# Kernel optimization log

Measured on AMD Instinct MI355X. Metric: run time of the kernel, lower is better.

Reference implementation:

```python
import jax, jax.numpy as jnp
import numpy as np

B, S, D, H = 8, 1024, 1024, 16
DK = D // H


def setup_inputs() -> dict:
    key = jax.random.key(0)
    ks = jax.random.split(key, 12)
    sc = 1.0 / np.sqrt(D)
    return {
        "query": jax.random.normal(ks[0], (B, S, D), jnp.float32),
        "key": jax.random.normal(ks[1], (B, S, D), jnp.float32),
        "value": jax.random.normal(ks[2], (B, S, D), jnp.float32),
        "Wq": jax.random.normal(ks[3], (D, D), jnp.float32) * sc,
        "bq": jnp.zeros((D,), jnp.float32),
        "Wk": jax.random.normal(ks[4], (D, D), jnp.float32) * sc,
        "bk": jnp.zeros((D,), jnp.float32),
        "Wv": jax.random.normal(ks[5], (D, D), jnp.float32) * sc,
        "bv": jnp.zeros((D,), jnp.float32),
        "Wa": jax.random.normal(ks[6], (D, D), jnp.float32) * sc,
        "ba": jnp.zeros((D,), jnp.float32),
        "qvec": jax.random.normal(ks[7], (D,), jnp.float32),
    }


def reference(query, key, value, Wq, bq, Wk, bk, Wv, bv, Wa, ba, qvec):
    # project and split heads: [B,S,D] -> [B,H,S,DK]
    def split(x, W, b):
        y = x @ W.T + b
        return y.reshape(B, S, H, DK).transpose(0, 2, 1, 3)

    q = split(query, Wq, bq)
    k = split(key, Wk, bk)
    v = split(value, Wv, bv)

    scores = jnp.einsum('bhqd,bhkd->bhqk', q, k) / jnp.sqrt(jnp.float32(DK))
    p = jax.nn.softmax(scores, axis=-1)          # dropout p=0 -> identity
    x = jnp.einsum('bhqk,bhkd->bhqd', p, v)
    x = x.transpose(0, 2, 1, 3).reshape(B, S, D)  # [B,S,D]

    # attention2 pooling head
    a = jnp.tanh(x @ Wa.T + ba) @ qvec           # [B,S]
    alpha = jax.nn.softmax(a, axis=-1)
    return jnp.einsum('bs,bsd->bd', alpha, x)    # [B,D]
```

## Files before the change

kernel.cpp:

```cpp
#include <hip/hip_runtime.h>

typedef __bf16 bf16;
typedef __attribute__((ext_vector_type(8))) __bf16 bf16x8;
typedef __attribute__((ext_vector_type(4))) __bf16 bf16x4;
typedef __attribute__((ext_vector_type(4))) float f32x4;

#define GLDS16(g, l) __builtin_amdgcn_global_load_lds( \
    (const __attribute__((address_space(1))) void*)(g), \
    (__attribute__((address_space(3))) void*)(l), 16, 0, 0)

#define MFMA16(a, b, c) __builtin_amdgcn_mfma_f32_16x16x32_bf16(a, b, c, 0, 0, 0)

#define TR16(dst, addr, off) \
  asm volatile("ds_read_b64_tr_b16 %0, %1 offset:" #off : "=v"(dst) : "v"(addr))

__global__ __launch_bounds__(256) void f2b_kernel(const float* __restrict__ in,
                                                  bf16* __restrict__ out, int n8) {
  int i = blockIdx.x * 256 + threadIdx.x;
  if (i >= n8) return;
  const f32x4* p = (const f32x4*)in + (size_t)i * 2;
  f32x4 a = p[0], b = p[1];
  bf16x8 o;
  o[0] = (bf16)a[0]; o[1] = (bf16)a[1]; o[2] = (bf16)a[2]; o[3] = (bf16)a[3];
  o[4] = (bf16)b[0]; o[5] = (bf16)b[1]; o[6] = (bf16)b[2]; o[7] = (bf16)b[3];
  ((bf16x8*)out)[i] = o;
}

template <int EPI>
__global__ __launch_bounds__(256) void gemm_bt(
    const bf16* __restrict__ A, const bf16* __restrict__ Bw,
    const float* __restrict__ bias, const float* __restrict__ qv,
    bf16* __restrict__ C, float* __restrict__ aout,
    int M, int N, int K) {
  __shared__ __attribute__((aligned(16))) bf16 As[4096];
  __shared__ __attribute__((aligned(16))) bf16 Bs[4096];
  const int tid = threadIdx.x;
  const int wid = tid >> 6, lane = tid & 63;
  const int g = lane >> 4, lc = lane & 15;
  const int row0 = blockIdx.x * 128, col0 = blockIdx.y * 128;
  const int wr = wid >> 1, wc = wid & 1;

  const int c0 = tid, c1 = tid + 256;
  const bf16* gA0 = A + ((size_t)(row0 + (c0 & 127)) * K + (c0 >> 7) * 8);
  const bf16* gA1 = A + ((size_t)(row0 + (c1 & 127)) * K + (c1 >> 7) * 8);
  const bf16* gB0 = Bw + ((size_t)(col0 + (c0 & 127)) * K + (c0 >> 7) * 8);
  const bf16* gB1 = Bw + ((size_t)(col0 + (c1 & 127)) * K + (c1 >> 7) * 8);
  bf16* lA0 = As + (size_t)(0 + wid * 64) * 8;
  bf16* lA1 = As + (size_t)(256 + wid * 64) * 8;
  bf16* lB0 = Bs + (size_t)(0 + wid * 64) * 8;
  bf16* lB1 = Bs + (size_t)(256 + wid * 64) * 8;

  const f32x4 z4 = {0.f, 0.f, 0.f, 0.f};
  f32x4 acc[4][4];
#pragma unroll
  for (int m = 0; m < 4; ++m)
#pragma unroll
    for (int n = 0; n < 4; ++n) acc[m][n] = z4;

  for (int kt = 0; kt < K; kt += 32) {
    GLDS16(gA0 + kt, lA0);
    GLDS16(gA1 + kt, lA1);
    GLDS16(gB0 + kt, lB0);
    GLDS16(gB1 + kt, lB1);
    __syncthreads();
    bf16x8 af[4], bfv[4];
#pragma unroll
    for (int m = 0; m < 4; ++m)
      af[m] = *(const bf16x8*)(As + g * 1024 + (wr * 64 + m * 16 + lc) * 8);
#pragma unroll
    for (int n = 0; n < 4; ++n)
      bfv[n] = *(const bf16x8*)(Bs + g * 1024 + (wc * 64 + n * 16 + lc) * 8);
#pragma unroll
    for (int m = 0; m < 4; ++m)
#pragma unroll
      for (int n = 0; n < 4; ++n)
        acc[m][n] = MFMA16(af[m], bfv[n], acc[m][n]);
    __syncthreads();
  }

  if constexpr (EPI == 0) {
#pragma unroll
    for (int n = 0; n < 4; ++n) {
      const int col = col0 + wc * 64 + n * 16 + lc;
      const float bb = bias[col];
#pragma unroll
      for (int m = 0; m < 4; ++m)
#pragma unroll
        for (int r = 0; r < 4; ++r) {
          const int row = row0 + wr * 64 + m * 16 + g * 4 + r;
          C[(size_t)row * N + col] = (bf16)(acc[m][n][r] + bb);
        }
    }
  } else {
    float part[4][4];
#pragma unroll
    for (int m = 0; m < 4; ++m)
#pragma unroll
      for (int r = 0; r < 4; ++r) part[m][r] = 0.f;
#pragma unroll
    for (int n = 0; n < 4; ++n) {
      const int col = col0 + wc * 64 + n * 16 + lc;
      const float bb = bias[col];
      const float qq = qv[col];
#pragma unroll
      for (int m = 0; m < 4; ++m)
#pragma unroll
        for (int r = 0; r < 4; ++r)
          part[m][r] += tanhf(acc[m][n][r] + bb) * qq;
    }
#pragma unroll
    for (int m = 0; m < 4; ++m)
#pragma unroll
      for (int r = 0; r < 4; ++r) {
        float v = part[m][r];
        v += __shfl_xor(v, 1); v += __shfl_xor(v, 2);
        v += __shfl_xor(v, 4); v += __shfl_xor(v, 8);
        if (lc == 0) {
          const int row = row0 + wr * 64 + m * 16 + g * 4 + r;
          atomicAdd(&aout[row], v);
        }
      }
  }
}

__global__ __launch_bounds__(256) void attn_kernel(
    const bf16* __restrict__ qp, const bf16* __restrict__ kp,
    const bf16* __restrict__ vp, bf16* __restrict__ xb, float* __restrict__ xf) {
  constexpr int S = 1024, D = 1024;
  __shared__ __attribute__((aligned(16))) bf16 Ks[4096];
  __shared__ __attribute__((aligned(16))) bf16 Vs[4096];
  __shared__ __attribute__((aligned(16))) bf16 Ps[4096];
  const int tid = threadIdx.x, wid = tid >> 6, lane = tid & 63;
  const int g = lane >> 4, lc = lane & 15;
  const int b = blockIdx.x >> 4, h = blockIdx.x & 15;
  const int q0 = blockIdx.y * 64;
  const size_t base = (size_t)b * S * D + (size_t)h * 64;

  bf16x8 qf[2];
  {
    const bf16* qrow = qp + base + (size_t)(q0 + wid * 16 + lc) * D;
    qf[0] = *(const bf16x8*)(qrow + g * 8);
    qf[1] = *(const bf16x8*)(qrow + 32 + g * 8);
#pragma unroll
    for (int j = 0; j < 8; ++j) {
      qf[0][j] = (bf16)((float)qf[0][j] * 0.125f);
      qf[1][j] = (bf16)((float)qf[1][j] * 0.125f);
    }
  }
  float m_s = -1e30f, l_s = 0.f;
  const f32x4 z4 = {0.f, 0.f, 0.f, 0.f};
  f32x4 ax[4];
#pragma unroll
  for (int m = 0; m < 4; ++m) ax[m] = z4;

  const int c0 = tid, c1 = tid + 256;
  const bf16* gK0 = kp + base + (size_t)(c0 & 63) * D + (c0 >> 6) * 8;
  const bf16* gK1 = kp + base + (size_t)(c1 & 63) * D + (c1 >> 6) * 8;
  bf16* lK0 = Ks + (size_t)(c0 - lane) * 8;
  bf16* lK1 = Ks + (size_t)(c1 - lane) * 8;
  const bf16* gV0 = vp + base + (size_t)((c0 >> 5) * 4 + ((c0 >> 1) & 3)) * D +
                    ((c0 >> 3) & 3) * 16 + (c0 & 1) * 8;
  const bf16* gV1 = vp + base + (size_t)((c1 >> 5) * 4 + ((c1 >> 1) & 3)) * D +
                    ((c1 >> 3) & 3) * 16 + (c1 & 1) * 8;
  bf16* lV0 = Vs + (size_t)(c0 - lane) * 8;
  bf16* lV1 = Vs + (size_t)(c1 - lane) * 8;

  bf16* pw = Ps + wid * 1024;
  const int pswz_a = lc & 3, pswz_b = (lc >> 2) & 3;
  const unsigned vaddr =
      (unsigned)(uintptr_t)(const __attribute__((address_space(3))) bf16*)(Vs + 512 * g + 4 * lc);

  for (int s0 = 0; s0 < S; s0 += 64) {
    __syncthreads();
    GLDS16(gK0 + (size_t)s0 * D, lK0);
    GLDS16(gK1 + (size_t)s0 * D, lK1);
    GLDS16(gV0 + (size_t)s0 * D, lV0);
    GLDS16(gV1 + (size_t)s0 * D, lV1);
    __syncthreads();

    f32x4 sc[4];
#pragma unroll
    for (int m = 0; m < 4; ++m) {
      f32x4 z = z4;
      bf16x8 kf0 = *(const bf16x8*)(Ks + (size_t)g * 512 + (m * 16 + lc) * 8);
      bf16x8 kf1 = *(const bf16x8*)(Ks + (size_t)(4 + g) * 512 + (m * 16 + lc) * 8);
      z = MFMA16(kf0, qf[0], z);
      z = MFMA16(kf1, qf[1], z);
      sc[m] = z;
    }
    float mx = -1e30f;
#pragma unroll
    for (int m = 0; m < 4; ++m)
      mx = fmaxf(mx, fmaxf(fmaxf(sc[m][0], sc[m][1]), fmaxf(sc[m][2], sc[m][3])));
    mx = fmaxf(mx, __shfl_xor(mx, 16));
    mx = fmaxf(mx, __shfl_xor(mx, 32));
    const float mn = fmaxf(m_s, mx);
    float sm = 0.f;
#pragma unroll
    for (int m = 0; m < 4; ++m)
#pragma unroll
      for (int r = 0; r < 4; ++r) {
        float p = __expf(sc[m][r] - mn);
        sc[m][r] = p;
        sm += p;
      }
    sm += __shfl_xor(sm, 16);
    sm += __shfl_xor(sm, 32);
    const float cr = __expf(m_s - mn);
    l_s = l_s * cr + sm;
    m_s = mn;

#pragma unroll
    for (int m = 0; m < 4; ++m) {
      bf16x4 pk;
      pk[0] = (bf16)sc[m][0]; pk[1] = (bf16)sc[m][1];
      pk[2] = (bf16)sc[m][2]; pk[3] = (bf16)sc[m][3];
      *(bf16x4*)(pw + lc * 64 + 16 * (m ^ pswz_a) + 4 * (g ^ pswz_b)) = pk;
    }
#pragma unroll
    for (int m = 0; m < 4; ++m) ax[m] *= cr;

    bf16x4 pr[2][2];
#pragma unroll
    for (int kk = 0; kk < 2; ++kk)
#pragma unroll
      for (int jh = 0; jh < 2; ++jh) {
        const int msrc = 2 * kk + (g >> 1);
        const int gsrc = (2 * g + jh) & 3;
        pr[kk][jh] = *(const bf16x4*)(pw + lc * 64 + 16 * (msrc ^ pswz_a) + 4 * (gsrc ^ pswz_b));
      }
    bf16x8 pf0 = __builtin_shufflevector(pr[0][0], pr[0][1], 0, 1, 2, 3, 4, 5, 6, 7);
    bf16x8 pf1 = __builtin_shufflevector(pr[1][0], pr[1][1], 0, 1, 2, 3, 4, 5, 6, 7);

    bf16x4 vt[4][2][2];
    TR16(vt[0][0][0], vaddr, 0);    TR16(vt[1][0][0], vaddr, 128);
    TR16(vt[2][0][0], vaddr, 256);  TR16(vt[3][0][0], vaddr, 384);
    TR16(vt[0][0][1], vaddr, 512);  TR16(vt[1][0][1], vaddr, 640);
    TR16(vt[2][0][1], vaddr, 768);  TR16(vt[3][0][1], vaddr, 896);
    TR16(vt[0][1][0], vaddr, 4096); TR16(vt[1][1][0], vaddr, 4224);
    TR16(vt[2][1][0], vaddr, 4352); TR16(vt[3][1][0], vaddr, 4480);
    TR16(vt[0][1][1], vaddr, 4608); TR16(vt[1][1][1], vaddr, 4736);
    TR16(vt[2][1][1], vaddr, 4864); TR16(vt[3][1][1], vaddr, 4992);
    asm volatile("s_waitcnt lgkmcnt(0)" ::: "memory");
    __builtin_amdgcn_sched_barrier(0);

#pragma unroll
    for (int md = 0; md < 4; ++md) {
      bf16x8 a0 = __builtin_shufflevector(vt[md][0][0], vt[md][0][1], 0, 1, 2, 3, 4, 5, 6, 7);
      bf16x8 a1 = __builtin_shufflevector(vt[md][1][0], vt[md][1][1], 0, 1, 2, 3, 4, 5, 6, 7);
      ax[md] = MFMA16(a0, pf0, ax[md]);
      ax[md] = MFMA16(a1, pf1, ax[md]);
    }
  }

  const float inv = 1.0f / l_s;
  const int qrow = q0 + wid * 16 + lc;
  float* xfr = xf + base + (size_t)qrow * D;
  bf16* xbr = xb + base + (size_t)qrow * D;
#pragma unroll
  for (int m = 0; m < 4; ++m)
#pragma unroll
    for (int r = 0; r < 4; ++r) {
      const int col = 16 * m + 4 * g + r;
      const float v = ax[m][r] * inv;
      xbr[col] = (bf16)v;
      xfr[col] = v;
    }
}

__global__ __launch_bounds__(256) void softmax_rows(const float* __restrict__ av,
                                                    float* __restrict__ alpha) {
  const int b = blockIdx.x, t = threadIdx.x;
  __shared__ float red[8];
  f32x4 v = *(const f32x4*)(av + b * 1024 + t * 4);
  float m = fmaxf(fmaxf(v[0], v[1]), fmaxf(v[2], v[3]));
#pragma unroll
  for (int o = 1; o < 64; o <<= 1) m = fmaxf(m, __shfl_xor(m, o));
  if ((t & 63) == 0) red[t >> 6] = m;
  __syncthreads();
  m = fmaxf(fmaxf(red[0], red[1]), fmaxf(red[2], red[3]));
  f32x4 e;
  float s = 0.f;
#pragma unroll
  for (int j = 0; j < 4; ++j) { e[j] = __expf(v[j] - m); s += e[j]; }
#pragma unroll
  for (int o = 1; o < 64; o <<= 1) s += __shfl_xor(s, o);
  if ((t & 63) == 0) red[4 + (t >> 6)] = s;
  __syncthreads();
  const float inv = 1.0f / (red[4] + red[5] + red[6] + red[7]);
  *(f32x4*)(alpha + b * 1024 + t * 4) = e * inv;
}

__global__ __launch_bounds__(256) void pool_kernel(const float* __restrict__ xf,
                                                   const float* __restrict__ alpha,
                                                   float* __restrict__ out) {
  const int b = blockIdx.y, sc = blockIdx.x, t = threadIdx.x;
  f32x4 acc = {0.f, 0.f, 0.f, 0.f};
  const float* xrow = xf + (size_t)b * 1024 * 1024;
  for (int s = sc * 64; s < sc * 64 + 64; ++s) {
    const float al = alpha[b * 1024 + s];
    f32x4 xv = *(const f32x4*)(xrow + (size_t)s * 1024 + t * 4);
    acc += xv * al;
  }
  atomicAdd(&out[b * 1024 + t * 4 + 0], acc[0]);
  atomicAdd(&out[b * 1024 + t * 4 + 1], acc[1]);
  atomicAdd(&out[b * 1024 + t * 4 + 2], acc[2]);
  atomicAdd(&out[b * 1024 + t * 4 + 3], acc[3]);
}

extern "C" void kernel_launch(void* const* d_in, const int* in_sizes, int n_in,
                              void* d_out, int out_size, void* d_ws, size_t ws_size,
                              hipStream_t stream) {
  const float* Q   = (const float*)d_in[0];
  const float* K   = (const float*)d_in[1];
  const float* V   = (const float*)d_in[2];
  const float* Wq  = (const float*)d_in[3];
  const float* bq  = (const float*)d_in[4];
  const float* Wk  = (const float*)d_in[5];
  const float* bk  = (const float*)d_in[6];
  const float* Wv  = (const float*)d_in[7];
  const float* bv  = (const float*)d_in[8];
  const float* Wa  = (const float*)d_in[9];
  const float* ba  = (const float*)d_in[10];
  const float* qvec = (const float*)d_in[11];
  float* out = (float*)d_out;
  char* ws = (char*)d_ws;
  const size_t MB = 1ull << 20;

  bf16* Wqb = (bf16*)(ws + 0 * MB);
  bf16* Wkb = (bf16*)(ws + 2 * MB);
  bf16* Wvb = (bf16*)(ws + 4 * MB);
  bf16* Wab = (bf16*)(ws + 6 * MB);
  bf16* qb  = (bf16*)(ws + 8 * MB);
  bf16* kb  = (bf16*)(ws + 24 * MB);
  bf16* vb  = (bf16*)(ws + 40 * MB);
  bf16* qp  = (bf16*)(ws + 56 * MB);
  bf16* kp  = (bf16*)(ws + 72 * MB);
  bf16* vp  = (bf16*)(ws + 88 * MB);
  float* av    = (float*)(ws + 104 * MB);
  float* alpha = (float*)(ws + 104 * MB + 65536);
  bf16* xb  = qb;
  float* xf = (float*)(ws + 24 * MB);

  f2b_kernel<<<4096, 256, 0, stream>>>(Q, qb, 1048576);
  f2b_kernel<<<4096, 256, 0, stream>>>(K, kb, 1048576);
  f2b_kernel<<<4096, 256, 0, stream>>>(V, vb, 1048576);
  f2b_kernel<<<512, 256, 0, stream>>>(Wq, Wqb, 131072);
  f2b_kernel<<<512, 256, 0, stream>>>(Wk, Wkb, 131072);
  f2b_kernel<<<512, 256, 0, stream>>>(Wv, Wvb, 131072);
  f2b_kernel<<<512, 256, 0, stream>>>(Wa, Wab, 131072);

  dim3 gg(64, 8);
  gemm_bt<0><<<gg, 256, 0, stream>>>(qb, Wqb, bq, nullptr, qp, nullptr, 8192, 1024, 1024);
  gemm_bt<0><<<gg, 256, 0, stream>>>(kb, Wkb, bk, nullptr, kp, nullptr, 8192, 1024, 1024);
  gemm_bt<0><<<gg, 256, 0, stream>>>(vb, Wvb, bv, nullptr, vp, nullptr, 8192, 1024, 1024);

  attn_kernel<<<dim3(128, 16), 256, 0, stream>>>(qp, kp, vp, xb, xf);

  hipMemsetAsync(av, 0, 8192 * sizeof(float), stream);
  gemm_bt<1><<<gg, 256, 0, stream>>>(xb, Wab, ba, qvec, nullptr, av, 8192, 1024, 1024);

  softmax_rows<<<8, 256, 0, stream>>>(av, alpha);

  hipMemsetAsync(out, 0, 8192 * sizeof(float), stream);
  pool_kernel<<<dim3(16, 8), 256, 0, stream>>>(xf, alpha, out);
}
```

Measured before the change: 282.0 us.

## Double-buffer GEMM and attention tiles, batch launches, lazy softmax rescale

Adds LDS double buffering to the GEMM and attention loops so the next tile's global-to-LDS load overlaps compute on the current tile, which also removes one barrier per iteration. Merges the seven conversion launches into two and the three projection GEMMs into one grid, and moves the memsets to the start. In attention it rescales the running max only when the max grows by more than a threshold, raises wave priority around MFMA blocks, and vectorizes output stores. The larger LDS footprint may reduce occupancy, and the lazy rescale lets exponentials exceed 1 by up to e^8.

Result: faster. 266.9 us (-5.3%).

```diff
diff --git a/kernel.cpp b/kernel.cpp
--- a/kernel.cpp
+++ b/kernel.cpp
@@ -14,26 +14,28 @@
 #define TR16(dst, addr, off) \
   asm volatile("ds_read_b64_tr_b16 %0, %1 offset:" #off : "=v"(dst) : "v"(addr))
 
-__global__ __launch_bounds__(256) void f2b_kernel(const float* __restrict__ in,
-                                                  bf16* __restrict__ out, int n8) {
+struct CvtArgs { const float* in[4]; bf16* out[4]; };
+
+__global__ __launch_bounds__(256) void f2b_multi(CvtArgs a, int n8) {
   int i = blockIdx.x * 256 + threadIdx.x;
   if (i >= n8) return;
+  const float* in = a.in[blockIdx.y];
+  bf16* out = a.out[blockIdx.y];
   const f32x4* p = (const f32x4*)in + (size_t)i * 2;
-  f32x4 a = p[0], b = p[1];
+  f32x4 x = p[0], y = p[1];
   bf16x8 o;
-  o[0] = (bf16)a[0]; o[1] = (bf16)a[1]; o[2] = (bf16)a[2]; o[3] = (bf16)a[3];
-  o[4] = (bf16)b[0]; o[5] = (bf16)b[1]; o[6] = (bf16)b[2]; o[7] = (bf16)b[3];
+  o[0] = (bf16)x[0]; o[1] = (bf16)x[1]; o[2] = (bf16)x[2]; o[3] = (bf16)x[3];
+  o[4] = (bf16)y[0]; o[5] = (bf16)y[1]; o[6] = (bf16)y[2]; o[7] = (bf16)y[3];
   ((bf16x8*)out)[i] = o;
 }
 
 template <int EPI>
-__global__ __launch_bounds__(256) void gemm_bt(
+__device__ __forceinline__ void gemm_body(
     const bf16* __restrict__ A, const bf16* __restrict__ Bw,
     const float* __restrict__ bias, const float* __restrict__ qv,
-    bf16* __restrict__ C, float* __restrict__ aout,
-    int M, int N, int K) {
-  __shared__ __attribute__((aligned(16))) bf16 As[4096];
-  __shared__ __attribute__((aligned(16))) bf16 Bs[4096];
+    bf16* __restrict__ C, float* __restrict__ aout, const int N, const int K) {
+  __shared__ __attribute__((aligned(16))) bf16 As[8192];
+  __shared__ __attribute__((aligned(16))) bf16 Bs[8192];
   const int tid = threadIdx.x;
   const int wid = tid >> 6, lane = tid & 63;
   const int g = lane >> 4, lc = lane & 15;
@@ -45,9 +47,9 @@
   const bf16* gA1 = A + ((size_t)(row0 + (c1 & 127)) * K + (c1 >> 7) * 8);
   const bf16* gB0 = Bw + ((size_t)(col0 + (c0 & 127)) * K + (c0 >> 7) * 8);
   const bf16* gB1 = Bw + ((size_t)(col0 + (c1 & 127)) * K + (c1 >> 7) * 8);
-  bf16* lA0 = As + (size_t)(0 + wid * 64) * 8;
+  bf16* lA0 = As + (size_t)(wid * 64) * 8;
   bf16* lA1 = As + (size_t)(256 + wid * 64) * 8;
-  bf16* lB0 = Bs + (size_t)(0 + wid * 64) * 8;
+  bf16* lB0 = Bs + (size_t)(wid * 64) * 8;
   bf16* lB1 = Bs + (size_t)(256 + wid * 64) * 8;
 
   const f32x4 z4 = {0.f, 0.f, 0.f, 0.f};
@@ -57,25 +59,35 @@
 #pragma unroll
     for (int n = 0; n < 4; ++n) acc[m][n] = z4;
 
+  GLDS16(gA0, lA0);
+  GLDS16(gA1, lA1);
+  GLDS16(gB0, lB0);
+  GLDS16(gB1, lB1);
+
   for (int kt = 0; kt < K; kt += 32) {
-    GLDS16(gA0 + kt, lA0);
-    GLDS16(gA1 + kt, lA1);
-    GLDS16(gB0 + kt, lB0);
-    GLDS16(gB1 + kt, lB1);
     __syncthreads();
+    const int cur = (kt >> 5) & 1;
+    if (kt + 32 < K) {
+      const int nb = cur ^ 1;
+      GLDS16(gA0 + kt + 32, lA0 + nb * 4096);
+      GLDS16(gA1 + kt + 32, lA1 + nb * 4096);
+      GLDS16(gB0 + kt + 32, lB0 + nb * 4096);
+      GLDS16(gB1 + kt + 32, lB1 + nb * 4096);
+    }
+    const bf16* Ab = As + cur * 4096;
+    const bf16* Bb = Bs + cur * 4096;
     bf16x8 af[4], bfv[4];
 #pragma unroll
     for (int m = 0; m < 4; ++m)
-      af[m] = *(const bf16x8*)(As + g * 1024 + (wr * 64 + m * 16 + lc) * 8);
+      af[m] = *(const bf16x8*)(Ab + g * 1024 + (wr * 64 + m * 16 + lc) * 8);
 #pragma unroll
     for (int n = 0; n < 4; ++n)
-      bfv[n] = *(const bf16x8*)(Bs + g * 1024 + (wc * 64 + n * 16 + lc) * 8);
+      bfv[n] = *(const bf16x8*)(Bb + g * 1024 + (wc * 64 + n * 16 + lc) * 8);
 #pragma unroll
     for (int m = 0; m < 4; ++m)
 #pragma unroll
       for (int n = 0; n < 4; ++n)
         acc[m][n] = MFMA16(af[m], bfv[n], acc[m][n]);
-    __syncthreads();
   }
 
   if constexpr (EPI == 0) {
@@ -123,12 +135,27 @@
   }
 }
 
+struct GemmSet { const bf16* A; const bf16* Bw; const float* bias; bf16* C; };
+struct Gemm3Args { GemmSet s[3]; };
+
+__global__ __launch_bounds__(256) void gemm3_kernel(Gemm3Args a) {
+  const GemmSet s = a.s[blockIdx.z];
+  gemm_body<0>(s.A, s.Bw, s.bias, nullptr, s.C, nullptr, 1024, 1024);
+}
+
+__global__ __launch_bounds__(256) void gemm_a_kernel(
+    const bf16* __restrict__ A, const bf16* __restrict__ Bw,
+    const float* __restrict__ bias, const float* __restrict__ qv,
+    float* __restrict__ aout) {
+  gemm_body<1>(A, Bw, bias, qv, nullptr, aout, 1024, 1024);
+}
+
 __global__ __launch_bounds__(256) void attn_kernel(
     const bf16* __restrict__ qp, const bf16* __restrict__ kp,
     const bf16* __restrict__ vp, bf16* __restrict__ xb, float* __restrict__ xf) {
   constexpr int S = 1024, D = 1024;
-  __shared__ __attribute__((aligned(16))) bf16 Ks[4096];
-  __shared__ __attribute__((aligned(16))) bf16 Vs[4096];
+  __shared__ __attribute__((aligned(16))) bf16 Ks[8192];
+  __shared__ __attribute__((aligned(16))) bf16 Vs[8192];
   __shared__ __attribute__((aligned(16))) bf16 Ps[4096];
   const int tid = threadIdx.x, wid = tid >> 6, lane = tid & 63;
   const int g = lane >> 4, lc = lane & 15;
@@ -167,48 +194,67 @@
 
   bf16* pw = Ps + wid * 1024;
   const int pswz_a = lc & 3, pswz_b = (lc >> 2) & 3;
-  const unsigned vaddr =
+  const unsigned vaddr0 =
       (unsigned)(uintptr_t)(const __attribute__((address_space(3))) bf16*)(Vs + 512 * g + 4 * lc);
 
-  for (int s0 = 0; s0 < S; s0 += 64) {
+  GLDS16(gK0, lK0);
+  GLDS16(gK1, lK1);
+  GLDS16(gV0, lV0);
+  GLDS16(gV1, lV1);
+
+  for (int t = 0; t < 16; ++t) {
     __syncthreads();
-    GLDS16(gK0 + (size_t)s0 * D, lK0);
-    GLDS16(gK1 + (size_t)s0 * D, lK1);
-    GLDS16(gV0 + (size_t)s0 * D, lV0);
-    GLDS16(gV1 + (size_t)s0 * D, lV1);
-    __syncthreads();
+    const int cur = t & 1;
+    if (t < 15) {
+      const size_t off = (size_t)(t + 1) * 64 * D;
+      const int nb = cur ^ 1;
+      GLDS16(gK0 + off, lK0 + nb * 4096);
+      GLDS16(gK1 + off, lK1 + nb * 4096);
+      GLDS16(gV0 + off, lV0 + nb * 4096);
+      GLDS16(gV1 + off, lV1 + nb * 4096);
+    }
+    const bf16* Kb = Ks + cur * 4096;
+    const unsigned va = vaddr0 + cur * 8192u;
 
     f32x4 sc[4];
+    __builtin_amdgcn_s_setprio(1);
 #pragma unroll
     for (int m = 0; m < 4; ++m) {
       f32x4 z = z4;
-      bf16x8 kf0 = *(const bf16x8*)(Ks + (size_t)g * 512 + (m * 16 + lc) * 8);
-      bf16x8 kf1 = *(const bf16x8*)(Ks + (size_t)(4 + g) * 512 + (m * 16 + lc) * 8);
+      bf16x8 kf0 = *(const bf16x8*)(Kb + (size_t)g * 512 + (m * 16 + lc) * 8);
+      bf16x8 kf1 = *(const bf16x8*)(Kb + (size_t)(4 + g) * 512 + (m * 16 + lc) * 8);
       z = MFMA16(kf0, qf[0], z);
       z = MFMA16(kf1, qf[1], z);
       sc[m] = z;
     }
+    __builtin_amdgcn_s_setprio(0);
+
     float mx = -1e30f;
 #pragma unroll
     for (int m = 0; m < 4; ++m)
       mx = fmaxf(mx, fmaxf(fmaxf(sc[m][0], sc[m][1]), fmaxf(sc[m][2], sc[m][3])));
     mx = fmaxf(mx, __shfl_xor(mx, 16));
     mx = fmaxf(mx, __shfl_xor(mx, 32));
-    const float mn = fmaxf(m_s, mx);
+    if (!__all(mx - m_s <= 8.f)) {
+      const float mn = fmaxf(m_s, mx);
+      const float cr = __expf(m_s - mn);
+      l_s *= cr;
+#pragma unroll
+      for (int m = 0; m < 4; ++m) ax[m] *= cr;
+      m_s = mn;
+    }
     float sm = 0.f;
 #pragma unroll
     for (int m = 0; m < 4; ++m)
 #pragma unroll
       for (int r = 0; r < 4; ++r) {
-        float p = __expf(sc[m][r] - mn);
+        float p = __expf(sc[m][r] - m_s);
         sc[m][r] = p;
         sm += p;
       }
     sm += __shfl_xor(sm, 16);
     sm += __shfl_xor(sm, 32);
-    const float cr = __expf(m_s - mn);
-    l_s = l_s * cr + sm;
-    m_s = mn;
+    l_s += sm;
 
 #pragma unroll
     for (int m = 0; m < 4; ++m) {
@@ -217,8 +263,6 @@
       pk[2] = (bf16)sc[m][2]; pk[3] = (bf16)sc[m][3];
       *(bf16x4*)(pw + lc * 64 + 16 * (m ^ pswz_a) + 4 * (g ^ pswz_b)) = pk;
     }
-#pragma unroll
-    for (int m = 0; m < 4; ++m) ax[m] *= cr;
 
     bf16x4 pr[2][2];
 #pragma unroll
@@ -233,17 +277,18 @@
     bf16x8 pf1 = __builtin_shufflevector(pr[1][0], pr[1][1], 0, 1, 2, 3, 4, 5, 6, 7);
 
     bf16x4 vt[4][2][2];
-    TR16(vt[0][0][0], vaddr, 0);    TR16(vt[1][0][0], vaddr, 128);
-    TR16(vt[2][0][0], vaddr, 256);  TR16(vt[3][0][0], vaddr, 384);
-    TR16(vt[0][0][1], vaddr, 512);  TR16(vt[1][0][1], vaddr, 640);
-    TR16(vt[2][0][1], vaddr, 768);  TR16(vt[3][0][1], vaddr, 896);
-    TR16(vt[0][1][0], vaddr, 4096); TR16(vt[1][1][0], vaddr, 4224);
-    TR16(vt[2][1][0], vaddr, 4352); TR16(vt[3][1][0], vaddr, 4480);
-    TR16(vt[0][1][1], vaddr, 4608); TR16(vt[1][1][1], vaddr, 4736);
-    TR16(vt[2][1][1], vaddr, 4864); TR16(vt[3][1][1], vaddr, 4992);
+    TR16(vt[0][0][0], va, 0);    TR16(vt[1][0][0], va, 128);
+    TR16(vt[2][0][0], va, 256);  TR16(vt[3][0][0], va, 384);
+    TR16(vt[0][0][1], va, 512);  TR16(vt[1][0][1], va, 640);
+    TR16(vt[2][0][1], va, 768);  TR16(vt[3][0][1], va, 896);
+    TR16(vt[0][1][0], va, 4096); TR16(vt[1][1][0], va, 4224);
+    TR16(vt[2][1][0], va, 4352); TR16(vt[3][1][0], va, 4480);
+    TR16(vt[0][1][1], va, 4608); TR16(vt[1][1][1], va, 4736);
+    TR16(vt[2][1][1], va, 4864); TR16(vt[3][1][1], va, 4992);
     asm volatile("s_waitcnt lgkmcnt(0)" ::: "memory");
     __builtin_amdgcn_sched_barrier(0);
 
+    __builtin_amdgcn_s_setprio(1);
 #pragma unroll
     for (int md = 0; md < 4; ++md) {
       bf16x8 a0 = __builtin_shufflevector(vt[md][0][0], vt[md][0][1], 0, 1, 2, 3, 4, 5, 6, 7);
@@ -251,6 +296,7 @@
       ax[md] = MFMA16(a0, pf0, ax[md]);
       ax[md] = MFMA16(a1, pf1, ax[md]);
     }
+    __builtin_amdgcn_s_setprio(0);
   }
 
   const float inv = 1.0f / l_s;
@@ -258,14 +304,14 @@
   float* xfr = xf + base + (size_t)qrow * D;
   bf16* xbr = xb + base + (size_t)qrow * D;
 #pragma unroll
-  for (int m = 0; m < 4; ++m)
-#pragma unroll
-    for (int r = 0; r < 4; ++r) {
-      const int col = 16 * m + 4 * g + r;
-      const float v = ax[m][r] * inv;
-      xbr[col] = (bf16)v;
-      xfr[col] = v;
-    }
+  for (int m = 0; m < 4; ++m) {
+    f32x4 vv = ax[m] * inv;
+    *(f32x4*)(xfr + 16 * m + 4 * g) = vv;
+    bf16x4 bb;
+    bb[0] = (bf16)vv[0]; bb[1] = (bf16)vv[1];
+    bb[2] = (bf16)vv[2]; bb[3] = (bf16)vv[3];
+    *(bf16x4*)(xbr + 16 * m + 4 * g) = bb;
+  }
 }
 
 __global__ __launch_bounds__(256) void softmax_rows(const float* __restrict__ av,
@@ -342,26 +388,21 @@
   bf16* xb  = qb;
   float* xf = (float*)(ws + 24 * MB);
 
-  f2b_kernel<<<4096, 256, 0, stream>>>(Q, qb, 1048576);
-  f2b_kernel<<<4096, 256, 0, stream>>>(K, kb, 1048576);
-  f2b_kernel<<<4096, 256, 0, stream>>>(V, vb, 1048576);
-  f2b_kernel<<<512, 256, 0, stream>>>(Wq, Wqb, 131072);
-  f2b_kernel<<<512, 256, 0, stream>>>(Wk, Wkb, 131072);
-  f2b_kernel<<<512, 256, 0, stream>>>(Wv, Wvb, 131072);
-  f2b_kernel<<<512, 256, 0, stream>>>(Wa, Wab, 131072);
-
-  dim3 gg(64, 8);
-  gemm_bt<0><<<gg, 256, 0, stream>>>(qb, Wqb, bq, nullptr, qp, nullptr, 8192, 1024, 1024);
-  gemm_bt<0><<<gg, 256, 0, stream>>>(kb, Wkb, bk, nullptr, kp, nullptr, 8192, 1024, 1024);
-  gemm_bt<0><<<gg, 256, 0, stream>>>(vb, Wvb, bv, nullptr, vp, nullptr, 8192, 1024, 1024);
+  hipMemsetAsync(av, 0, 8192 * sizeof(float), stream);
+  hipMemsetAsync(out, 0, 8192 * sizeof(float), stream);
+
+  CvtArgs cq = {{Q, K, V, nullptr}, {qb, kb, vb, nullptr}};
+  f2b_multi<<<dim3(4096, 3), 256, 0, stream>>>(cq, 1048576);
+  CvtArgs cw = {{Wq, Wk, Wv, Wa}, {Wqb, Wkb, Wvb, Wab}};
+  f2b_multi<<<dim3(512, 4), 256, 0, stream>>>(cw, 131072);
+
+  Gemm3Args g3 = {{{qb, Wqb, bq, qp}, {kb, Wkb, bk, kp}, {vb, Wvb, bv, vp}}};
+  gemm3_kernel<<<dim3(64, 8, 3), 256, 0, stream>>>(g3);
 
   attn_kernel<<<dim3(128, 16), 256, 0, stream>>>(qp, kp, vp, xb, xf);
 
-  hipMemsetAsync(av, 0, 8192 * sizeof(float), stream);
-  gemm_bt<1><<<gg, 256, 0, stream>>>(xb, Wab, ba, qvec, nullptr, av, 8192, 1024, 1024);
+  gemm_a_kernel<<<dim3(64, 8), 256, 0, stream>>>(xb, Wab, ba, qvec, av);
 
   softmax_rows<<<8, 256, 0, stream>>>(av, alpha);
-
-  hipMemsetAsync(out, 0, 8192 * sizeof(float), stream);
   pool_kernel<<<dim3(16, 8), 256, 0, stream>>>(xf, alpha, out);
 }
```
